# Kernel optimization log

Hardware: AMD Instinct MI355X
Metric: run time of the kernel (lower is better)

Reference implementation:

```python
import jax, jax.numpy as jnp
import numpy as np

V, C, COUT, DEG = 50000, 128, 256, 16
E = V * DEG


def setup_inputs() -> dict:
    key = jax.random.key(0)
    k1, k2, k3, k4 = jax.random.split(key, 4)
    data = jax.random.normal(k1, (V, C), dtype=jnp.float32)
    # Every vertex gets exactly DEG neighbors -> sorted segment ids.
    edge_src = jnp.repeat(jnp.arange(V, dtype=jnp.int32), DEG)
    edge_dst = jax.random.randint(k2, (E,), 0, V, dtype=jnp.int32)
    # Row-normalized neighbor weights (sum over each vertex's edges == 1).
    raw_w = jax.random.uniform(k3, (E,), dtype=jnp.float32) + 0.1
    row_sum = jax.ops.segment_sum(raw_w, edge_src, num_segments=V)
    edge_w = raw_w / row_sum[edge_src]
    kernel = jax.random.normal(k4, (2 * C, COUT), dtype=jnp.float32) * (1.0 / np.sqrt(2 * C))
    bias = jnp.zeros((COUT,), dtype=jnp.float32)
    return {"data": data, "edge_src": edge_src, "edge_dst": edge_dst,
            "edge_w": edge_w, "kernel": kernel, "bias": bias}


def reference(data, edge_src, edge_dst, edge_w, kernel, bias):
    # Gather per-edge endpoint features: x = data[i], y = data[j].
    x = data[edge_src]                       # [E, C]
    y = data[edge_dst]                       # [E, C]
    # Edge function h(x, y) = Linear([x, y - x]) (1x1 Conv1D, no activation).
    feat = jnp.concatenate([x, y - x], axis=-1)          # [E, 2C]
    edge_out = feat @ kernel + bias                       # [E, COUT]
    # reduction='weighted': out[i] = sum_j w_ij * h(x_i, x_j).
    out = jax.ops.segment_sum(edge_w[:, None] * edge_out, edge_src,
                              num_segments=data.shape[0])  # [V, COUT]
    return out
```

## Files before the change

### kernel.cpp

```cpp
#include <hip/hip_runtime.h>
#include <hip/hip_bf16.h>
#include <cstdint>

#define V_N    50000
#define C_N    128
#define COUT_N 256
#define DEG_N  16
#define K2_N   256

typedef short bf16x8 __attribute__((ext_vector_type(8)));
typedef float f32x4  __attribute__((ext_vector_type(4)));

__device__ __forceinline__ unsigned short f2bf(float f) {
    union { float f; unsigned u; } a; a.f = f;
    unsigned r = a.u + 0x7fffu + ((a.u >> 16) & 1u);
    return (unsigned short)(r >> 16);
}
__device__ __forceinline__ float bf2f(unsigned h) {
    union { unsigned u; float f; } a; a.u = h << 16; return a.f;
}

__global__ void prep_bt_kernel(const float* __restrict__ kern,
                               unsigned short* __restrict__ bt) {
    const int k = blockIdx.x;
    const int n = threadIdx.x;
    bt[n * K2_N + k] = f2bf(kern[k * COUT_N + n]);
}

__global__ __launch_bounds__(256)
void prep_data_kernel(const float* __restrict__ data,
                      unsigned short* __restrict__ db) {
    const int i = blockIdx.x * 256 + threadIdx.x;
    const float4 f0 = *reinterpret_cast<const float4*>(data + (size_t)i * 8);
    const float4 f1 = *reinterpret_cast<const float4*>(data + (size_t)i * 8 + 4);
    union { unsigned short h[8]; uint4 q; } o;
    o.h[0] = f2bf(f0.x); o.h[1] = f2bf(f0.y); o.h[2] = f2bf(f0.z); o.h[3] = f2bf(f0.w);
    o.h[4] = f2bf(f1.x); o.h[5] = f2bf(f1.y); o.h[6] = f2bf(f1.z); o.h[7] = f2bf(f1.w);
    *reinterpret_cast<uint4*>(db + (size_t)i * 8) = o.q;
}

__global__ __launch_bounds__(256, 4)
void dgc_fused_kernel(const unsigned short* __restrict__ db,
                      const int* __restrict__ edge_dst,
                      const float* __restrict__ edge_w,
                      const unsigned short* __restrict__ btg,
                      const float* __restrict__ bias,
                      float* __restrict__ out) {
    __shared__ __align__(16) char Asm[64 * 512];

    const int tid  = threadIdx.x;
    const int lane = tid & 63;
    const int wid  = __builtin_amdgcn_readfirstlane(tid >> 6);
    const int m0   = blockIdx.x * 64;

    #pragma unroll 2
    for (int t = 0; t < 16; ++t) {
        const int row = wid * 16 + t;
        const int vtx = m0 + row;
        float ux = 0.f, uy = 0.f, vx = 0.f, vy = 0.f;
        if (vtx < V_N) {
            const int*   __restrict__ dst = edge_dst + vtx * DEG_N;
            const float* __restrict__ ww  = edge_w  + vtx * DEG_N;
            float sx = 0.f, sy = 0.f, Wsum = 0.f;
            #pragma unroll
            for (int k = 0; k < DEG_N; ++k) {
                const float wk = ww[k];
                const int   j  = dst[k];
                const unsigned p = *reinterpret_cast<const unsigned*>(
                    db + (size_t)j * C_N + lane * 2);
                sx = fmaf(wk, bf2f(p & 0xffffu), sx);
                sy = fmaf(wk, bf2f(p >> 16), sy);
                Wsum += wk;
            }
            const unsigned xp = *reinterpret_cast<const unsigned*>(
                db + (size_t)vtx * C_N + lane * 2);
            ux = Wsum * bf2f(xp & 0xffffu);
            uy = Wsum * bf2f(xp >> 16);
            vx = sx - ux;
            vy = sy - uy;
        }
        const unsigned up = (unsigned)f2bf(ux) | ((unsigned)f2bf(uy) << 16);
        const unsigned vp = (unsigned)f2bf(vx) | ((unsigned)f2bf(vy) << 16);
        const int sw     = row & 7;
        const int cu     = lane >> 2;
        const int within = (lane & 3) * 4;
        char* rowp = Asm + row * 512;
        *reinterpret_cast<unsigned*>(rowp + ((cu        ^ sw) * 16 + within)) = up;
        *reinterpret_cast<unsigned*>(rowp + (((16 + cu) ^ sw) * 16 + within)) = vp;
    }
    __syncthreads();

    const int wm = wid >> 1;
    const int wn = wid & 1;

    #pragma unroll
    for (int h = 0; h < 2; ++h) {
        f32x4 acc[2][4];
        #pragma unroll
        for (int mf = 0; mf < 2; ++mf)
            #pragma unroll
            for (int nf = 0; nf < 4; ++nf)
                acc[mf][nf] = (f32x4){0.f, 0.f, 0.f, 0.f};

        #pragma unroll
        for (int ks = 0; ks < 8; ++ks) {
            bf16x8 a[2], b[4];
            #pragma unroll
            for (int mf = 0; mf < 2; ++mf) {
                const int r  = wm * 32 + mf * 16 + (lane & 15);
                const int ck = (ks * 4 + (lane >> 4)) ^ (r & 7);
                a[mf] = *reinterpret_cast<const bf16x8*>(Asm + r * 512 + ck * 16);
            }
            #pragma unroll
            for (int nf = 0; nf < 4; ++nf) {
                const int n = h * 128 + wn * 64 + nf * 16 + (lane & 15);
                b[nf] = *reinterpret_cast<const bf16x8*>(
                    btg + (size_t)n * K2_N + (ks * 4 + (lane >> 4)) * 8);
            }
            #pragma unroll
            for (int mf = 0; mf < 2; ++mf)
                #pragma unroll
                for (int nf = 0; nf < 4; ++nf)
                    acc[mf][nf] = __builtin_amdgcn_mfma_f32_16x16x32_bf16(
                        a[mf], b[nf], acc[mf][nf], 0, 0, 0);
        }

        #pragma unroll
        for (int mf = 0; mf < 2; ++mf) {
            const int row_l = wm * 32 + mf * 16 + (lane >> 4) * 4;
            #pragma unroll
            for (int nf = 0; nf < 4; ++nf) {
                const int col = h * 128 + wn * 64 + nf * 16 + (lane & 15);
                const float bb = bias[col];
                #pragma unroll
                for (int r = 0; r < 4; ++r) {
                    const int rg = m0 + row_l + r;
                    if (rg < V_N)
                        out[(size_t)rg * COUT_N + col] = acc[mf][nf][r] + bb;
                }
            }
        }
    }
}

extern "C" void kernel_launch(void* const* d_in, const int* in_sizes, int n_in,
                              void* d_out, int out_size, void* d_ws, size_t ws_size,
                              hipStream_t stream) {
    const float* data     = (const float*)d_in[0];
    const int*   edge_dst = (const int*)d_in[2];
    const float* edge_w   = (const float*)d_in[3];
    const float* kern     = (const float*)d_in[4];
    const float* bias     = (const float*)d_in[5];
    float*       out      = (float*)d_out;

    unsigned short* bt = (unsigned short*)d_ws;
    unsigned short* db = (unsigned short*)d_ws + (size_t)K2_N * COUT_N;

    prep_bt_kernel<<<K2_N, COUT_N, 0, stream>>>(kern, bt);
    prep_data_kernel<<<(V_N * C_N / 8) / 256, 256, 0, stream>>>(data, db);

    const int nblk = (V_N + 63) / 64;
    dgc_fused_kernel<<<nblk, 256, 0, stream>>>(db, edge_dst, edge_w, bt, bias, out);
}
```

Baseline: 150.3 us.

## Widen gather to 16B loads, pre-tile weights, double block to 512 threads

The gather phase now has each 16-lane group handle one vertex with 16-byte loads of 8 bf16 channels, so four vertices are processed per wave at a time instead of one row of 4-byte loads. The weight matrix is rearranged in the prep kernel into an MFMA fragment-ordered layout so B loads are contiguous, and the block grows to 8 waves. This split removes the two-pass N loop, since each wave now covers a 32x64 output tile. The aim is fewer, wider gather transactions and more memory-level parallelism, at the cost of higher register pressure under launch bounds of 512 threads with 6 blocks.

```diff
diff --git a/kernel.cpp b/kernel.cpp
--- a/kernel.cpp
+++ b/kernel.cpp
@@ -16,15 +16,20 @@
     unsigned r = a.u + 0x7fffu + ((a.u >> 16) & 1u);
     return (unsigned short)(r >> 16);
 }
-__device__ __forceinline__ float bf2f(unsigned h) {
-    union { unsigned u; float f; } a; a.u = h << 16; return a.f;
+__device__ __forceinline__ float bflo(unsigned p) {
+    union { unsigned u; float f; } a; a.u = p << 16; return a.f;
+}
+__device__ __forceinline__ float bfhi(unsigned p) {
+    union { unsigned u; float f; } a; a.u = p & 0xffff0000u; return a.f;
 }
 
 __global__ void prep_bt_kernel(const float* __restrict__ kern,
                                unsigned short* __restrict__ bt) {
     const int k = blockIdx.x;
     const int n = threadIdx.x;
-    bt[n * K2_N + k] = f2bf(kern[k * COUT_N + n]);
+    const int idx = (((n >> 4) * 8 + (k >> 5)) * 4 + ((k >> 3) & 3)) * 128
+                  + (n & 15) * 8 + (k & 7);
+    bt[idx] = f2bf(kern[k * COUT_N + n]);
 }
 
 __global__ __launch_bounds__(256)
@@ -39,7 +44,7 @@
     *reinterpret_cast<uint4*>(db + (size_t)i * 8) = o.q;
 }
 
-__global__ __launch_bounds__(256, 4)
+__global__ __launch_bounds__(512, 6)
 void dgc_fused_kernel(const unsigned short* __restrict__ db,
                       const int* __restrict__ edge_dst,
                       const float* __restrict__ edge_w,
@@ -52,92 +57,108 @@
     const int lane = tid & 63;
     const int wid  = __builtin_amdgcn_readfirstlane(tid >> 6);
     const int m0   = blockIdx.x * 64;
+    const int g    = lane >> 4;
+    const int c    = lane & 15;
 
-    #pragma unroll 2
-    for (int t = 0; t < 16; ++t) {
-        const int row = wid * 16 + t;
-        const int vtx = m0 + row;
-        float ux = 0.f, uy = 0.f, vx = 0.f, vy = 0.f;
-        if (vtx < V_N) {
-            const int*   __restrict__ dst = edge_dst + vtx * DEG_N;
-            const float* __restrict__ ww  = edge_w  + vtx * DEG_N;
-            float sx = 0.f, sy = 0.f, Wsum = 0.f;
+    #pragma unroll
+    for (int q = 0; q < 2; ++q) {
+        const int row = wid * 8 + q * 4 + g;
+        const int vq  = m0 + row;
+        float s[8];
+        #pragma unroll
+        for (int i = 0; i < 8; ++i) s[i] = 0.f;
+        float Wsum = 0.f;
+        uint4 xr = make_uint4(0u, 0u, 0u, 0u);
+        if (vq < V_N) {
+            xr = *reinterpret_cast<const uint4*>(db + (size_t)vq * C_N + c * 8);
+            const int eb = vq * DEG_N;
             #pragma unroll
             for (int k = 0; k < DEG_N; ++k) {
-                const float wk = ww[k];
-                const int   j  = dst[k];
-                const unsigned p = *reinterpret_cast<const unsigned*>(
-                    db + (size_t)j * C_N + lane * 2);
-                sx = fmaf(wk, bf2f(p & 0xffffu), sx);
-                sy = fmaf(wk, bf2f(p >> 16), sy);
+                const int   j  = edge_dst[eb + k];
+                const float wk = edge_w[eb + k];
+                const uint4 r  = *reinterpret_cast<const uint4*>(
+                    db + (size_t)j * C_N + c * 8);
+                s[0] = fmaf(wk, bflo(r.x), s[0]);
+                s[1] = fmaf(wk, bfhi(r.x), s[1]);
+                s[2] = fmaf(wk, bflo(r.y), s[2]);
+                s[3] = fmaf(wk, bfhi(r.y), s[3]);
+                s[4] = fmaf(wk, bflo(r.z), s[4]);
+                s[5] = fmaf(wk, bfhi(r.z), s[5]);
+                s[6] = fmaf(wk, bflo(r.w), s[6]);
+                s[7] = fmaf(wk, bfhi(r.w), s[7]);
                 Wsum += wk;
             }
-            const unsigned xp = *reinterpret_cast<const unsigned*>(
-                db + (size_t)vtx * C_N + lane * 2);
-            ux = Wsum * bf2f(xp & 0xffffu);
-            uy = Wsum * bf2f(xp >> 16);
-            vx = sx - ux;
-            vy = sy - uy;
         }
-        const unsigned up = (unsigned)f2bf(ux) | ((unsigned)f2bf(uy) << 16);
-        const unsigned vp = (unsigned)f2bf(vx) | ((unsigned)f2bf(vy) << 16);
-        const int sw     = row & 7;
-        const int cu     = lane >> 2;
-        const int within = (lane & 3) * 4;
-        char* rowp = Asm + row * 512;
-        *reinterpret_cast<unsigned*>(rowp + ((cu        ^ sw) * 16 + within)) = up;
-        *reinterpret_cast<unsigned*>(rowp + (((16 + cu) ^ sw) * 16 + within)) = vp;
+        float u[8], v[8];
+        u[0] = Wsum * bflo(xr.x); u[1] = Wsum * bfhi(xr.x);
+        u[2] = Wsum * bflo(xr.y); u[3] = Wsum * bfhi(xr.y);
+        u[4] = Wsum * bflo(xr.z); u[5] = Wsum * bfhi(xr.z);
+        u[6] = Wsum * bflo(xr.w); u[7] = Wsum * bfhi(xr.w);
+        #pragma unroll
+        for (int i = 0; i < 8; ++i) v[i] = s[i] - u[i];
+
+        uint4 up, vp;
+        up.x = (unsigned)f2bf(u[0]) | ((unsigned)f2bf(u[1]) << 16);
+        up.y = (unsigned)f2bf(u[2]) | ((unsigned)f2bf(u[3]) << 16);
+        up.z = (unsigned)f2bf(u[4]) | ((unsigned)f2bf(u[5]) << 16);
+        up.w = (unsigned)f2bf(u[6]) | ((unsigned)f2bf(u[7]) << 16);
+        vp.x = (unsigned)f2bf(v[0]) | ((unsigned)f2bf(v[1]) << 16);
+        vp.y = (unsigned)f2bf(v[2]) | ((unsigned)f2bf(v[3]) << 16);
+        vp.z = (unsigned)f2bf(v[4]) | ((unsigned)f2bf(v[5]) << 16);
+        vp.w = (unsigned)f2bf(v[6]) | ((unsigned)f2bf(v[7]) << 16);
+
+        const int sw   = row & 7;
+        char*     rowp = Asm + row * 512;
+        *reinterpret_cast<uint4*>(rowp + ((c        ^ sw) * 16)) = up;
+        *reinterpret_cast<uint4*>(rowp + (((16 + c) ^ sw) * 16)) = vp;
     }
     __syncthreads();
 
-    const int wm = wid >> 1;
-    const int wn = wid & 1;
+    const int wm = wid >> 2;
+    const int wn = wid & 3;
+
+    f32x4 acc[2][4];
+    #pragma unroll
+    for (int mf = 0; mf < 2; ++mf)
+        #pragma unroll
+        for (int nf = 0; nf < 4; ++nf)
+            acc[mf][nf] = (f32x4){0.f, 0.f, 0.f, 0.f};
 
     #pragma unroll
-    for (int h = 0; h < 2; ++h) {
-        f32x4 acc[2][4];
+    for (int ks = 0; ks < 8; ++ks) {
+        bf16x8 a[2], b[4];
+        #pragma unroll
+        for (int mf = 0; mf < 2; ++mf) {
+            const int r  = wm * 32 + mf * 16 + c;
+            const int ck = (ks * 4 + g) ^ (r & 7);
+            a[mf] = *reinterpret_cast<const bf16x8*>(Asm + r * 512 + ck * 16);
+        }
+        #pragma unroll
+        for (int nf = 0; nf < 4; ++nf) {
+            const int nb = wn * 4 + nf;
+            b[nf] = *reinterpret_cast<const bf16x8*>(
+                btg + (size_t)((nb * 32 + ks * 4 + g) * 16 + c) * 8);
+        }
         #pragma unroll
         for (int mf = 0; mf < 2; ++mf)
             #pragma unroll
             for (int nf = 0; nf < 4; ++nf)
-                acc[mf][nf] = (f32x4){0.f, 0.f, 0.f, 0.f};
+                acc[mf][nf] = __builtin_amdgcn_mfma_f32_16x16x32_bf16(
+                    a[mf], b[nf], acc[mf][nf], 0, 0, 0);
+    }
 
+    #pragma unroll
+    for (int mf = 0; mf < 2; ++mf) {
+        const int row_l = wm * 32 + mf * 16 + g * 4;
         #pragma unroll
-        for (int ks = 0; ks < 8; ++ks) {
-            bf16x8 a[2], b[4];
+        for (int nf = 0; nf < 4; ++nf) {
+            const int col = wn * 64 + nf * 16 + c;
+            const float bb = bias[col];
             #pragma unroll
-            for (int mf = 0; mf < 2; ++mf) {
-                const int r  = wm * 32 + mf * 16 + (lane & 15);
-                const int ck = (ks * 4 + (lane >> 4)) ^ (r & 7);
-                a[mf] = *reinterpret_cast<const bf16x8*>(Asm + r * 512 + ck * 16);
-            }
-            #pragma unroll
-            for (int nf = 0; nf < 4; ++nf) {
-                const int n = h * 128 + wn * 64 + nf * 16 + (lane & 15);
-                b[nf] = *reinterpret_cast<const bf16x8*>(
-                    btg + (size_t)n * K2_N + (ks * 4 + (lane >> 4)) * 8);
-            }
-            #pragma unroll
-            for (int mf = 0; mf < 2; ++mf)
-                #pragma unroll
-                for (int nf = 0; nf < 4; ++nf)
-                    acc[mf][nf] = __builtin_amdgcn_mfma_f32_16x16x32_bf16(
-                        a[mf], b[nf], acc[mf][nf], 0, 0, 0);
-        }
-
-        #pragma unroll
-        for (int mf = 0; mf < 2; ++mf) {
-            const int row_l = wm * 32 + mf * 16 + (lane >> 4) * 4;
-            #pragma unroll
-            for (int nf = 0; nf < 4; ++nf) {
-                const int col = h * 128 + wn * 64 + nf * 16 + (lane & 15);
-                const float bb = bias[col];
-                #pragma unroll
-                for (int r = 0; r < 4; ++r) {
-                    const int rg = m0 + row_l + r;
-                    if (rg < V_N)
-                        out[(size_t)rg * COUT_N + col] = acc[mf][nf][r] + bb;
-                }
+            for (int r = 0; r < 4; ++r) {
+                const int rg = m0 + row_l + r;
+                if (rg < V_N)
+                    out[(size_t)rg * COUT_N + col] = acc[mf][nf][r] + bb;
             }
         }
     }
@@ -160,5 +181,5 @@
     prep_data_kernel<<<(V_N * C_N / 8) / 256, 256, 0, stream>>>(data, db);
 
     const int nblk = (V_N + 63) / 64;
-    dgc_fused_kernel<<<nblk, 256, 0, stream>>>(db, edge_dst, edge_w, bt, bias, out);
+    dgc_fused_kernel<<<nblk, 512, 0, stream>>>(db, edge_dst, edge_w, bt, bias, out);
 }
```

Result: slower. 182.2 us (+21.2%).
